# Kernel optimization log

Hardware: AMD Instinct MI355X
Metric: run time of the kernel (lower is better)

## Reference

```python
import jax, jax.numpy as jnp
import numpy as np

POINT_DIM, VOXEL_DIM, NUM_HEADS = 3, 256, 8
HEAD_DIM = VOXEL_DIM // NUM_HEADS


def _linear_params(key, fan_in, fan_out):
    kw, kb = jax.random.split(key)
    bound = 1.0 / np.sqrt(fan_in)
    W = jax.random.uniform(kw, (fan_out, fan_in), jnp.float32, -bound, bound)
    b = jax.random.uniform(kb, (fan_out,), jnp.float32, -bound, bound)
    return W, b


def setup_inputs() -> dict:
    key = jax.random.key(0)
    ks = jax.random.split(key, 7)
    points = jax.random.normal(ks[0], (2, 4096, POINT_DIM), jnp.float32)
    voxel_features = jax.random.normal(ks[1], (2, 2048, VOXEL_DIM), jnp.float32)
    Wp, bp = _linear_params(ks[2], POINT_DIM, VOXEL_DIM)
    Wq, bq = _linear_params(ks[3], VOXEL_DIM, VOXEL_DIM)
    Wk, bk = _linear_params(ks[4], VOXEL_DIM, VOXEL_DIM)
    Wv, bv = _linear_params(ks[5], VOXEL_DIM, VOXEL_DIM)
    Wf, bf = _linear_params(ks[6], VOXEL_DIM * 2, VOXEL_DIM)
    return {
        "points": points, "voxel_features": voxel_features,
        "Wp": Wp, "bp": bp, "Wq": Wq, "bq": bq,
        "Wk": Wk, "bk": bk, "Wv": Wv, "bv": bv,
        "Wf": Wf, "bf": bf,
    }


def reference(points, voxel_features, Wp, bp, Wq, bq, Wk, bk, Wv, bv, Wf, bf):
    B, N, _ = points.shape
    M = voxel_features.shape[1]
    # projections (torch Linear: x @ W.T + b)
    point_features = points @ Wp.T + bp                      # [B,N,D]
    q = (point_features @ Wq.T + bq).reshape(B, N, NUM_HEADS, HEAD_DIM)
    k = (voxel_features @ Wk.T + bk).reshape(B, M, NUM_HEADS, HEAD_DIM)
    v = (voxel_features @ Wv.T + bv).reshape(B, M, NUM_HEADS, HEAD_DIM)
    # attention scores [B,H,N,M]
    scale = 1.0 / np.sqrt(HEAD_DIM).astype(np.float32)
    attn = jnp.einsum('bnhd,bmhd->bhnm', q, k) * scale
    attn = jax.nn.softmax(attn, axis=-1)
    attended = jnp.einsum('bhnm,bmhd->bnhd', attn, v).reshape(B, N, VOXEL_DIM)
    fused = jnp.concatenate([point_features, attended], axis=-1) @ Wf.T + bf
    return fused
```

## Files before the change

### kernel.cpp

```cpp
#include <hip/hip_runtime.h>

#define B_ 2
#define N_ 4096
#define M_ 2048
#define D_ 256
#define H_ 8
#define DH_ 32
#define ROWS_ (B_*N_)
#define KVROWS_ (B_*M_)
#define PRE_ (0.17677669529663687f * 1.4426950408889634f)
#define CBASE_ 32.0f

typedef __attribute__((ext_vector_type(8))) short short8_t;
typedef __attribute__((ext_vector_type(4))) float float4_t;

#if defined(__has_builtin)
# if __has_builtin(__builtin_amdgcn_exp2f)
#  define EXP2F(x) __builtin_amdgcn_exp2f(x)
# else
#  define EXP2F(x) exp2f(x)
# endif
#else
# define EXP2F(x) exp2f(x)
#endif

__device__ __forceinline__ unsigned int rne_u(float f) {
    union { float f; unsigned int u; } c;
    c.f = f;
    return c.u + 0x7FFFu + ((c.u >> 16) & 1u);
}

__device__ __forceinline__ unsigned short f2us(float f) {
    return (unsigned short)(rne_u(f) >> 16);
}

__device__ __forceinline__ unsigned int pack2rn(float a, float b) {
    return __builtin_amdgcn_perm(rne_u(b), rne_u(a), 0x07060302u);
}

__device__ __forceinline__ unsigned int pack2tr(float a, float b) {
    union { float f; unsigned int u; } x, y;
    x.f = a; y.f = b;
    return __builtin_amdgcn_perm(y.u, x.u, 0x07060302u);
}

__device__ __forceinline__ short8_t cvt8(float4 a, float4 b) {
    union { unsigned int u[4]; short8_t s; } c;
    c.u[0] = pack2rn(a.x, a.y);
    c.u[1] = pack2rn(a.z, a.w);
    c.u[2] = pack2rn(b.x, b.y);
    c.u[3] = pack2rn(b.z, b.w);
    return c.s;
}

__device__ __forceinline__ int xcd_swz(int bid, int nwg) {
    const int cpx = nwg >> 3;
    return (bid & 7) * cpx + (bid >> 3);
}

template<int K, int NCOL>
__device__ __forceinline__ void stageB(const float* __restrict__ W, int col0,
                                       unsigned short* __restrict__ Bs, int tid)
{
    const int n = tid & (NCOL - 1), g = tid / NCOL;
    const int GROUPS = 256 / NCOL;
    const int CPT = (K / 8) / GROUPS;
    const float* src = W + (size_t)(col0 + n) * K + g * (K / GROUPS);
#pragma unroll
    for (int ci = 0; ci < CPT; ci++) {
        int logc = g * CPT + ci;
        int phys = logc ^ (n & 7);
        short8_t v = cvt8(*(const float4*)(src + ci * 8), *(const float4*)(src + ci * 8 + 4));
        *(short8_t*)(Bs + (size_t)n * K + phys * 8) = v;
    }
}

template<int K>
__device__ __forceinline__ short8_t readB(const unsigned short* __restrict__ Bs,
                                          int c, int l16, int quad, int k0)
{
    int phys = ((k0 >> 3) + quad) ^ (l16 & 7);
    return *(const short8_t*)(Bs + (size_t)(16 * c + l16) * K + phys * 8);
}

__global__ __launch_bounds__(256) void g_proj(
    const float* __restrict__ points, const float* __restrict__ voxel,
    const float* __restrict__ Wp, const float* __restrict__ bp,
    const float* __restrict__ Wq, const float* __restrict__ bq,
    const float* __restrict__ Wk, const float* __restrict__ bk,
    const float* __restrict__ Wv, const float* __restrict__ bv,
    unsigned short* __restrict__ pf_g, unsigned short* __restrict__ q_g,
    unsigned short* __restrict__ k_g, unsigned short* __restrict__ vt_g)
{
    const int tid = threadIdx.x;
    const int wave = tid >> 6, lane = tid & 63, quad = lane >> 4, l16 = lane & 15;

    __shared__ unsigned short Bs[64 * 256];
    __shared__ float Wp_lds[256 * 5];

    if (blockIdx.x < 512) {
        const int row0 = ((int)blockIdx.x >> 2) * 64;
        const int col0 = ((int)blockIdx.x & 3) * 64;
        stageB<256, 64>(Wq, col0, Bs, tid);
        Wp_lds[tid * 5 + 0] = Wp[tid * 3 + 0];
        Wp_lds[tid * 5 + 1] = Wp[tid * 3 + 1];
        Wp_lds[tid * 5 + 2] = Wp[tid * 3 + 2];
        Wp_lds[tid * 5 + 3] = bp[tid];
        __syncthreads();

        const int n = row0 + wave * 16 + l16;
        const float p0 = points[(size_t)n * 3 + 0];
        const float p1 = points[(size_t)n * 3 + 1];
        const float p2 = points[(size_t)n * 3 + 2];

        float4_t acc[4];
#pragma unroll
        for (int c = 0; c < 4; c++) acc[c] = (float4_t){0.f, 0.f, 0.f, 0.f};

#pragma unroll
        for (int k0 = 0; k0 < 256; k0 += 32) {
            float pf[8];
#pragma unroll
            for (int j = 0; j < 8; j++) {
                int c = k0 + quad * 8 + j;
                pf[j] = p0 * Wp_lds[c * 5 + 0] + p1 * Wp_lds[c * 5 + 1]
                      + p2 * Wp_lds[c * 5 + 2] + Wp_lds[c * 5 + 3];
            }
            short8_t af = cvt8(make_float4(pf[0], pf[1], pf[2], pf[3]),
                               make_float4(pf[4], pf[5], pf[6], pf[7]));
            if (col0 == 0)
                *(short8_t*)(pf_g + (size_t)n * D_ + k0 + quad * 8) = af;
#pragma unroll
            for (int c = 0; c < 4; c++)
                acc[c] = __builtin_amdgcn_mfma_f32_16x16x32_bf16(af, readB<256>(Bs, c, l16, quad, k0), acc[c], 0, 0, 0);
        }
#pragma unroll
        for (int c = 0; c < 4; c++) {
            int col = col0 + 16 * c + l16;
            float bb = bq[col];
#pragma unroll
            for (int r = 0; r < 4; r++) {
                int row = row0 + wave * 16 + quad * 4 + r;
                q_g[(size_t)row * D_ + col] = f2us((acc[c][r] + bb) * PRE_);
            }
        }
    } else {
        const int bid = (int)blockIdx.x - 512;
        const int row0 = (bid >> 2) * 64;
        const int col0 = (bid & 3) * 64;
        const float* arow = voxel + (size_t)(row0 + wave * 16 + l16) * D_;

        float4_t ak[4], av[4];
#pragma unroll
        for (int c = 0; c < 4; c++) {
            ak[c] = (float4_t){0.f, 0.f, 0.f, 0.f};
            av[c] = (float4_t){0.f, 0.f, 0.f, 0.f};
        }
        stageB<256, 64>(Wk, col0, Bs, tid);
        __syncthreads();
#pragma unroll
        for (int k0 = 0; k0 < 256; k0 += 32) {
            short8_t af = cvt8(*(const float4*)(arow + k0 + quad * 8),
                               *(const float4*)(arow + k0 + quad * 8 + 4));
#pragma unroll
            for (int c = 0; c < 4; c++)
                ak[c] = __builtin_amdgcn_mfma_f32_16x16x32_bf16(af, readB<256>(Bs, c, l16, quad, k0), ak[c], 0, 0, 0);
        }
        __syncthreads();
        stageB<256, 64>(Wv, col0, Bs, tid);
        __syncthreads();
#pragma unroll
        for (int k0 = 0; k0 < 256; k0 += 32) {
            short8_t af = cvt8(*(const float4*)(arow + k0 + quad * 8),
                               *(const float4*)(arow + k0 + quad * 8 + 4));
#pragma unroll
            for (int c = 0; c < 4; c++)
                av[c] = __builtin_amdgcn_mfma_f32_16x16x32_bf16(af, readB<256>(Bs, c, l16, quad, k0), av[c], 0, 0, 0);
        }
        const int b = row0 / M_;
        const int m0 = row0 - b * M_ + wave * 16 + quad * 4;
#pragma unroll
        for (int c = 0; c < 4; c++) {
            int col = col0 + 16 * c + l16;
            float bbk = bk[col], bbv = bv[col];
#pragma unroll
            for (int r = 0; r < 4; r++) {
                int row = row0 + wave * 16 + quad * 4 + r;
                k_g[(size_t)row * D_ + col] = f2us(ak[c][r] + bbk);
            }
            int h = col >> 5, dh = col & 31;
            unsigned int u0 = pack2rn(av[c][0] + bbv, av[c][1] + bbv);
            unsigned int u1 = pack2rn(av[c][2] + bbv, av[c][3] + bbv);
            *(uint2*)(vt_g + (size_t)((b * H_ + h) * DH_ + dh) * M_ + m0) = make_uint2(u0, u1);
        }
    }
}

__global__ __launch_bounds__(256) void k_attn6(
    const unsigned short* __restrict__ q_g,
    const unsigned short* __restrict__ k_g,
    const unsigned short* __restrict__ vt_g,
    unsigned short* __restrict__ att_g)
{
    const int tid = threadIdx.x;
    const int w = tid >> 6, lane = tid & 63, quad = lane >> 4, l16 = lane & 15;
    const int lbid = xcd_swz((int)blockIdx.x, B_ * H_ * (N_ / 64));
    const int nt = lbid & 63;
    const int bh = lbid >> 6;
    const int b = bh >> 3, h = bh & 7;
    const int n0 = nt * 64 + w * 16;

    __shared__ unsigned short Kt[2][64][40];
    __shared__ unsigned short Vt[2][32][72];
    __shared__ unsigned short Pb[4][16][64];

    short8_t qf = *(const short8_t*)(q_g + (size_t)(b * N_ + n0 + l16) * D_ + h * DH_ + quad * 8);

    float4_t od0 = {0.f, 0.f, 0.f, 0.f};
    float4_t od1 = {0.f, 0.f, 0.f, 0.f};
    float l_lane = 0.f;

    const unsigned short* kbase = k_g + (size_t)(b * M_) * D_ + h * DH_;
    const unsigned short* vbase = vt_g + (size_t)(bh * DH_) * M_;
    unsigned short* pb = &Pb[w][0][0];
    const int h7 = l16 & 7;
    const float4_t zc = {-CBASE_, -CBASE_, -CBASE_, -CBASE_};

    const int kr = tid >> 2, kc = tid & 3;
    const int vr = tid >> 3, vc = tid & 7;

    *(short8_t*)&Kt[0][kr][kc * 8] = *(const short8_t*)(kbase + (size_t)kr * D_ + kc * 8);
    *(short8_t*)&Vt[0][vr][vc * 8] = *(const short8_t*)(vbase + (size_t)vr * M_ + vc * 8);

    for (int s = 0; s < M_ / 64; s++) {
        __syncthreads();
        const int buf = s & 1;
        if (s + 1 < M_ / 64) {
            const int kv1 = (s + 1) * 64;
            *(short8_t*)&Kt[buf ^ 1][kr][kc * 8] =
                *(const short8_t*)(kbase + (size_t)(kv1 + kr) * D_ + kc * 8);
            *(short8_t*)&Vt[buf ^ 1][vr][vc * 8] =
                *(const short8_t*)(vbase + (size_t)vr * M_ + kv1 + vc * 8);
        }

        float4_t st[4];
#pragma unroll
        for (int t = 0; t < 4; t++) {
            short8_t kf = *(const short8_t*)&Kt[buf][16 * t + l16][quad * 8];
            st[t] = __builtin_amdgcn_mfma_f32_16x16x32_bf16(kf, qf, zc, 0, 0, 0);
        }

        float psum = 0.f;
#pragma unroll
        for (int t = 0; t < 4; t++) {
            float p0 = EXP2F(st[t][0]);
            float p1 = EXP2F(st[t][1]);
            float p2 = EXP2F(st[t][2]);
            float p3 = EXP2F(st[t][3]);
            psum += (p0 + p1) + (p2 + p3);
            unsigned int u0 = pack2tr(p0, p1);
            unsigned int u1 = pack2tr(p2, p3);
            int phys = (2 * t + (quad >> 1)) ^ h7;
            *(uint2*)(pb + l16 * 64 + phys * 8 + (quad & 1) * 4) = make_uint2(u0, u1);
        }
        l_lane += psum;

        short8_t pfa = *(const short8_t*)(pb + l16 * 64 + (quad ^ h7) * 8);
        short8_t pfb = *(const short8_t*)(pb + l16 * 64 + ((4 + quad) ^ h7) * 8);

        short8_t vf00 = *(const short8_t*)&Vt[buf][l16][quad * 8];
        short8_t vf01 = *(const short8_t*)&Vt[buf][l16][32 + quad * 8];
        short8_t vf10 = *(const short8_t*)&Vt[buf][16 + l16][quad * 8];
        short8_t vf11 = *(const short8_t*)&Vt[buf][16 + l16][32 + quad * 8];
        od0 = __builtin_amdgcn_mfma_f32_16x16x32_bf16(vf00, pfa, od0, 0, 0, 0);
        od0 = __builtin_amdgcn_mfma_f32_16x16x32_bf16(vf01, pfb, od0, 0, 0, 0);
        od1 = __builtin_amdgcn_mfma_f32_16x16x32_bf16(vf10, pfa, od1, 0, 0, 0);
        od1 = __builtin_amdgcn_mfma_f32_16x16x32_bf16(vf11, pfb, od1, 0, 0, 0);
    }

    l_lane += __shfl_xor(l_lane, 16);
    l_lane += __shfl_xor(l_lane, 32);
    const float inv = 1.0f / l_lane;

    unsigned short* ob = att_g + (size_t)(b * N_ + n0 + l16) * D_ + h * DH_;
    {
        unsigned int u0 = pack2rn(od0[0] * inv, od0[1] * inv);
        unsigned int u1 = pack2rn(od0[2] * inv, od0[3] * inv);
        *(uint2*)(ob + quad * 4) = make_uint2(u0, u1);
        unsigned int u2 = pack2rn(od1[0] * inv, od1[1] * inv);
        unsigned int u3 = pack2rn(od1[2] * inv, od1[3] * inv);
        *(uint2*)(ob + 16 + quad * 4) = make_uint2(u2, u3);
    }
}

__global__ __launch_bounds__(256) void g_fuse(
    const unsigned short* __restrict__ pf_g,
    const unsigned short* __restrict__ att_g,
    const float* __restrict__ Wf, const float* __restrict__ bfb,
    float* __restrict__ out)
{
    const int tid = threadIdx.x;
    const int wave = tid >> 6, lane = tid & 63, quad = lane >> 4, l16 = lane & 15;
    const int lbid = xcd_swz((int)blockIdx.x, (ROWS_ / 64) * 8);
    const int row0 = (lbid >> 3) * 64;
    const int col0 = (lbid & 7) * 32;

    __shared__ unsigned short Bs[32 * 512];

    stageB<512, 32>(Wf, col0, Bs, tid);
    __syncthreads();

    float4_t acc[2];
#pragma unroll
    for (int c = 0; c < 2; c++) acc[c] = (float4_t){0.f, 0.f, 0.f, 0.f};

    const size_t arow = (size_t)(row0 + wave * 16 + l16) * D_;
#pragma unroll
    for (int k0 = 0; k0 < 512; k0 += 32) {
        const unsigned short* xsrc = (k0 < 256) ? (pf_g + arow + k0) : (att_g + arow + (k0 - 256));
        short8_t af = *(const short8_t*)(xsrc + quad * 8);
#pragma unroll
        for (int c = 0; c < 2; c++)
            acc[c] = __builtin_amdgcn_mfma_f32_16x16x32_bf16(af, readB<512>(Bs, c, l16, quad, k0), acc[c], 0, 0, 0);
    }
#pragma unroll
    for (int c = 0; c < 2; c++) {
        int col = col0 + 16 * c + l16;
        float bb = bfb[col];
#pragma unroll
        for (int r = 0; r < 4; r++) {
            int row = row0 + wave * 16 + quad * 4 + r;
            out[(size_t)row * D_ + col] = acc[c][r] + bb;
        }
    }
}

extern "C" void kernel_launch(void* const* d_in, const int* in_sizes, int n_in,
                              void* d_out, int out_size, void* d_ws, size_t ws_size,
                              hipStream_t stream)
{
    const float* points = (const float*)d_in[0];
    const float* voxel  = (const float*)d_in[1];
    const float* Wp  = (const float*)d_in[2];
    const float* bp  = (const float*)d_in[3];
    const float* Wq  = (const float*)d_in[4];
    const float* bq  = (const float*)d_in[5];
    const float* Wk  = (const float*)d_in[6];
    const float* bk  = (const float*)d_in[7];
    const float* Wv  = (const float*)d_in[8];
    const float* bv  = (const float*)d_in[9];
    const float* Wf  = (const float*)d_in[10];
    const float* bfb = (const float*)d_in[11];
    float* out = (float*)d_out;

    unsigned short* ws = (unsigned short*)d_ws;
    unsigned short* pf_g  = ws;
    unsigned short* q_g   = pf_g  + (size_t)ROWS_ * D_;
    unsigned short* k_g   = q_g   + (size_t)ROWS_ * D_;
    unsigned short* vt_g  = k_g   + (size_t)KVROWS_ * D_;
    unsigned short* att_g = vt_g  + (size_t)KVROWS_ * D_;

    g_proj <<<dim3(768),  dim3(256), 0, stream>>>(points, voxel, Wp, bp, Wq, bq,
                                                  Wk, bk, Wv, bv, pf_g, q_g, k_g, vt_g);
    k_attn6<<<dim3(B_ * H_ * (N_ / 64)), dim3(256), 0, stream>>>(q_g, k_g, vt_g, att_g);
    g_fuse <<<dim3((ROWS_ / 64) * 8), dim3(256), 0, stream>>>(pf_g, att_g, Wf, bfb, out);
}
```

Measured before the change: 159.7 us.

## Fold point projection into Wq and Wf, compute q inside attention

```diff
diff --git a/kernel.cpp b/kernel.cpp
--- a/kernel.cpp
+++ b/kernel.cpp
@@ -58,14 +58,14 @@
     return (bid & 7) * cpx + (bid >> 3);
 }
 
-template<int K, int NCOL>
-__device__ __forceinline__ void stageB(const float* __restrict__ W, int col0,
-                                       unsigned short* __restrict__ Bs, int tid)
+template<int K, int NCOL, int LDSRC>
+__device__ __forceinline__ void stageB2(const float* __restrict__ W, int col0, int kof,
+                                        unsigned short* __restrict__ Bs, int tid)
 {
     const int n = tid & (NCOL - 1), g = tid / NCOL;
     const int GROUPS = 256 / NCOL;
     const int CPT = (K / 8) / GROUPS;
-    const float* src = W + (size_t)(col0 + n) * K + g * (K / GROUPS);
+    const float* src = W + (size_t)(col0 + n) * LDSRC + kof + g * (K / GROUPS);
 #pragma unroll
     for (int ci = 0; ci < CPT; ci++) {
         int logc = g * CPT + ci;
@@ -83,99 +83,47 @@
     return *(const short8_t*)(Bs + (size_t)(16 * c + l16) * K + phys * 8);
 }
 
-__global__ __launch_bounds__(256) void g_proj(
-    const float* __restrict__ points, const float* __restrict__ voxel,
+__global__ __launch_bounds__(256) void g_projkv(
+    const float* __restrict__ voxel,
     const float* __restrict__ Wp, const float* __restrict__ bp,
     const float* __restrict__ Wq, const float* __restrict__ bq,
     const float* __restrict__ Wk, const float* __restrict__ bk,
     const float* __restrict__ Wv, const float* __restrict__ bv,
-    unsigned short* __restrict__ pf_g, unsigned short* __restrict__ q_g,
-    unsigned short* __restrict__ k_g, unsigned short* __restrict__ vt_g)
+    const float* __restrict__ Wf, const float* __restrict__ bfb,
+    unsigned short* __restrict__ k_g, unsigned short* __restrict__ vt_g,
+    float* __restrict__ Wqc, float* __restrict__ Wfc)
 {
     const int tid = threadIdx.x;
     const int wave = tid >> 6, lane = tid & 63, quad = lane >> 4, l16 = lane & 15;
 
     __shared__ unsigned short Bs[64 * 256];
-    __shared__ float Wp_lds[256 * 5];
-
-    if (blockIdx.x < 512) {
-        const int row0 = ((int)blockIdx.x >> 2) * 64;
-        const int col0 = ((int)blockIdx.x & 3) * 64;
-        stageB<256, 64>(Wq, col0, Bs, tid);
-        Wp_lds[tid * 5 + 0] = Wp[tid * 3 + 0];
-        Wp_lds[tid * 5 + 1] = Wp[tid * 3 + 1];
-        Wp_lds[tid * 5 + 2] = Wp[tid * 3 + 2];
-        Wp_lds[tid * 5 + 3] = bp[tid];
-        __syncthreads();
-
-        const int n = row0 + wave * 16 + l16;
-        const float p0 = points[(size_t)n * 3 + 0];
-        const float p1 = points[(size_t)n * 3 + 1];
-        const float p2 = points[(size_t)n * 3 + 2];
-
-        float4_t acc[4];
-#pragma unroll
-        for (int c = 0; c < 4; c++) acc[c] = (float4_t){0.f, 0.f, 0.f, 0.f};
-
-#pragma unroll
-        for (int k0 = 0; k0 < 256; k0 += 32) {
-            float pf[8];
-#pragma unroll
-            for (int j = 0; j < 8; j++) {
-                int c = k0 + quad * 8 + j;
-                pf[j] = p0 * Wp_lds[c * 5 + 0] + p1 * Wp_lds[c * 5 + 1]
-                      + p2 * Wp_lds[c * 5 + 2] + Wp_lds[c * 5 + 3];
-            }
-            short8_t af = cvt8(make_float4(pf[0], pf[1], pf[2], pf[3]),
-                               make_float4(pf[4], pf[5], pf[6], pf[7]));
-            if (col0 == 0)
-                *(short8_t*)(pf_g + (size_t)n * D_ + k0 + quad * 8) = af;
-#pragma unroll
-            for (int c = 0; c < 4; c++)
-                acc[c] = __builtin_amdgcn_mfma_f32_16x16x32_bf16(af, readB<256>(Bs, c, l16, quad, k0), acc[c], 0, 0, 0);
-        }
-#pragma unroll
-        for (int c = 0; c < 4; c++) {
-            int col = col0 + 16 * c + l16;
-            float bb = bq[col];
-#pragma unroll
-            for (int r = 0; r < 4; r++) {
-                int row = row0 + wave * 16 + quad * 4 + r;
-                q_g[(size_t)row * D_ + col] = f2us((acc[c][r] + bb) * PRE_);
-            }
-        }
-    } else {
-        const int bid = (int)blockIdx.x - 512;
+    __shared__ unsigned short Bs2[64 * 256];
+
+    if (blockIdx.x < 256) {
+        const int bid = (int)blockIdx.x;
         const int row0 = (bid >> 2) * 64;
         const int col0 = (bid & 3) * 64;
         const float* arow = voxel + (size_t)(row0 + wave * 16 + l16) * D_;
 
+        stageB2<256, 64, 256>(Wk, col0, 0, Bs, tid);
+        stageB2<256, 64, 256>(Wv, col0, 0, Bs2, tid);
+
         float4_t ak[4], av[4];
 #pragma unroll
         for (int c = 0; c < 4; c++) {
             ak[c] = (float4_t){0.f, 0.f, 0.f, 0.f};
             av[c] = (float4_t){0.f, 0.f, 0.f, 0.f};
         }
-        stageB<256, 64>(Wk, col0, Bs, tid);
         __syncthreads();
 #pragma unroll
         for (int k0 = 0; k0 < 256; k0 += 32) {
             short8_t af = cvt8(*(const float4*)(arow + k0 + quad * 8),
                                *(const float4*)(arow + k0 + quad * 8 + 4));
 #pragma unroll
-            for (int c = 0; c < 4; c++)
-                ak[c] = __builtin_amdgcn_mfma_f32_16x16x32_bf16(af, readB<256>(Bs, c, l16, quad, k0), ak[c], 0, 0, 0);
-        }
-        __syncthreads();
-        stageB<256, 64>(Wv, col0, Bs, tid);
-        __syncthreads();
-#pragma unroll
-        for (int k0 = 0; k0 < 256; k0 += 32) {
-            short8_t af = cvt8(*(const float4*)(arow + k0 + quad * 8),
-                               *(const float4*)(arow + k0 + quad * 8 + 4));
-#pragma unroll
-            for (int c = 0; c < 4; c++)
-                av[c] = __builtin_amdgcn_mfma_f32_16x16x32_bf16(af, readB<256>(Bs, c, l16, quad, k0), av[c], 0, 0, 0);
+            for (int c = 0; c < 4; c++) {
+                ak[c] = __builtin_amdgcn_mfma_f32_16x16x32_bf16(af, readB<256>(Bs,  c, l16, quad, k0), ak[c], 0, 0, 0);
+                av[c] = __builtin_amdgcn_mfma_f32_16x16x32_bf16(af, readB<256>(Bs2, c, l16, quad, k0), av[c], 0, 0, 0);
+            }
         }
         const int b = row0 / M_;
         const int m0 = row0 - b * M_ + wave * 16 + quad * 4;
@@ -193,11 +141,39 @@
             unsigned int u1 = pack2rn(av[c][2] + bbv, av[c][3] + bbv);
             *(uint2*)(vt_g + (size_t)((b * H_ + h) * DH_ + dh) * M_ + m0) = make_uint2(u0, u1);
         }
-    }
-}
-
-__global__ __launch_bounds__(256) void k_attn6(
-    const unsigned short* __restrict__ q_g,
+    } else {
+        const int role = (int)blockIdx.x - 256;
+        float* wps = (float*)Bs;
+        *(float4*)(wps + tid * 4) = make_float4(Wp[tid * 3 + 0], Wp[tid * 3 + 1],
+                                                Wp[tid * 3 + 2], bp[tid]);
+        __syncthreads();
+        const int col = tid;
+        const float* wrow = role ? (Wf + (size_t)col * 512) : (Wq + (size_t)col * 256);
+        float a0 = 0.f, a1 = 0.f, a2 = 0.f, ab = 0.f;
+#pragma unroll 4
+        for (int d = 0; d < 256; d += 4) {
+            float4 wv = *(const float4*)(wrow + d);
+            float4 w0 = *(const float4*)(wps + (d + 0) * 4);
+            float4 w1 = *(const float4*)(wps + (d + 1) * 4);
+            float4 w2 = *(const float4*)(wps + (d + 2) * 4);
+            float4 w3 = *(const float4*)(wps + (d + 3) * 4);
+            a0 += wv.x * w0.x + wv.y * w1.x + wv.z * w2.x + wv.w * w3.x;
+            a1 += wv.x * w0.y + wv.y * w1.y + wv.z * w2.y + wv.w * w3.y;
+            a2 += wv.x * w0.z + wv.y * w1.z + wv.z * w2.z + wv.w * w3.z;
+            ab += wv.x * w0.w + wv.y * w1.w + wv.z * w2.w + wv.w * w3.w;
+        }
+        if (role == 0) {
+            *(float4*)(Wqc + (size_t)col * 4) =
+                make_float4(a0 * PRE_, a1 * PRE_, a2 * PRE_, (ab + bq[col]) * PRE_);
+        } else {
+            *(float4*)(Wfc + (size_t)col * 4) =
+                make_float4(a0, a1, a2, ab + bfb[col]);
+        }
+    }
+}
+
+__global__ __launch_bounds__(256) void k_attn7(
+    const float* __restrict__ points, const float* __restrict__ Wqc,
     const unsigned short* __restrict__ k_g,
     const unsigned short* __restrict__ vt_g,
     unsigned short* __restrict__ att_g)
@@ -214,52 +190,66 @@
     __shared__ unsigned short Vt[2][32][72];
     __shared__ unsigned short Pb[4][16][64];
 
-    short8_t qf = *(const short8_t*)(q_g + (size_t)(b * N_ + n0 + l16) * D_ + h * DH_ + quad * 8);
+    const unsigned short* kbase = k_g + (size_t)(b * M_) * D_ + h * DH_;
+    const unsigned short* vbase = vt_g + (size_t)(bh * DH_) * M_;
+
+    const int kr = tid >> 2, kc = tid & 3;
+    const int vr = tid >> 3, vc = tid & 7;
+
+    *(short8_t*)&Kt[0][kr][kc * 8] = *(const short8_t*)(kbase + (size_t)kr * D_ + kc * 8);
+    *(short8_t*)&Vt[0][vr][vc * 8] = *(const short8_t*)(vbase + (size_t)vr * M_ + vc * 8);
+
+    const size_t qrow = (size_t)(b * N_ + n0 + l16);
+    const float p0 = points[qrow * 3 + 0];
+    const float p1 = points[qrow * 3 + 1];
+    const float p2 = points[qrow * 3 + 2];
+    float q8[8];
+#pragma unroll
+    for (int j = 0; j < 8; j++) {
+        float4 wc = *(const float4*)(Wqc + (size_t)(h * DH_ + quad * 8 + j) * 4);
+        q8[j] = p0 * wc.x + p1 * wc.y + p2 * wc.z + wc.w;
+    }
+    short8_t qf = cvt8(make_float4(q8[0], q8[1], q8[2], q8[3]),
+                       make_float4(q8[4], q8[5], q8[6], q8[7]));
 
     float4_t od0 = {0.f, 0.f, 0.f, 0.f};
     float4_t od1 = {0.f, 0.f, 0.f, 0.f};
     float l_lane = 0.f;
 
-    const unsigned short* kbase = k_g + (size_t)(b * M_) * D_ + h * DH_;
-    const unsigned short* vbase = vt_g + (size_t)(bh * DH_) * M_;
     unsigned short* pb = &Pb[w][0][0];
     const int h7 = l16 & 7;
     const float4_t zc = {-CBASE_, -CBASE_, -CBASE_, -CBASE_};
 
-    const int kr = tid >> 2, kc = tid & 3;
-    const int vr = tid >> 3, vc = tid & 7;
-
-    *(short8_t*)&Kt[0][kr][kc * 8] = *(const short8_t*)(kbase + (size_t)kr * D_ + kc * 8);
-    *(short8_t*)&Vt[0][vr][vc * 8] = *(const short8_t*)(vbase + (size_t)vr * M_ + vc * 8);
-
     for (int s = 0; s < M_ / 64; s++) {
         __syncthreads();
         const int buf = s & 1;
-        if (s + 1 < M_ / 64) {
+        const bool more = (s + 1 < M_ / 64);
+        short8_t knext, vnext;
+        if (more) {
             const int kv1 = (s + 1) * 64;
-            *(short8_t*)&Kt[buf ^ 1][kr][kc * 8] =
-                *(const short8_t*)(kbase + (size_t)(kv1 + kr) * D_ + kc * 8);
-            *(short8_t*)&Vt[buf ^ 1][vr][vc * 8] =
-                *(const short8_t*)(vbase + (size_t)vr * M_ + kv1 + vc * 8);
+            knext = *(const short8_t*)(kbase + (size_t)(kv1 + kr) * D_ + kc * 8);
+            vnext = *(const short8_t*)(vbase + (size_t)vr * M_ + kv1 + vc * 8);
         }
 
         float4_t st[4];
+        __builtin_amdgcn_s_setprio(1);
 #pragma unroll
         for (int t = 0; t < 4; t++) {
             short8_t kf = *(const short8_t*)&Kt[buf][16 * t + l16][quad * 8];
             st[t] = __builtin_amdgcn_mfma_f32_16x16x32_bf16(kf, qf, zc, 0, 0, 0);
         }
+        __builtin_amdgcn_s_setprio(0);
 
         float psum = 0.f;
 #pragma unroll
         for (int t = 0; t < 4; t++) {
-            float p0 = EXP2F(st[t][0]);
-            float p1 = EXP2F(st[t][1]);
-            float p2 = EXP2F(st[t][2]);
-            float p3 = EXP2F(st[t][3]);
-            psum += (p0 + p1) + (p2 + p3);
-            unsigned int u0 = pack2tr(p0, p1);
-            unsigned int u1 = pack2tr(p2, p3);
+            float p0e = EXP2F(st[t][0]);
+            float p1e = EXP2F(st[t][1]);
+            float p2e = EXP2F(st[t][2]);
+            float p3e = EXP2F(st[t][3]);
+            psum += (p0e + p1e) + (p2e + p3e);
+            unsigned int u0 = pack2tr(p0e, p1e);
+            unsigned int u1 = pack2tr(p2e, p3e);
             int phys = (2 * t + (quad >> 1)) ^ h7;
             *(uint2*)(pb + l16 * 64 + phys * 8 + (quad & 1) * 4) = make_uint2(u0, u1);
         }
@@ -272,10 +262,17 @@
         short8_t vf01 = *(const short8_t*)&Vt[buf][l16][32 + quad * 8];
         short8_t vf10 = *(const short8_t*)&Vt[buf][16 + l16][quad * 8];
         short8_t vf11 = *(const short8_t*)&Vt[buf][16 + l16][32 + quad * 8];
+        __builtin_amdgcn_s_setprio(1);
         od0 = __builtin_amdgcn_mfma_f32_16x16x32_bf16(vf00, pfa, od0, 0, 0, 0);
         od0 = __builtin_amdgcn_mfma_f32_16x16x32_bf16(vf01, pfb, od0, 0, 0, 0);
         od1 = __builtin_amdgcn_mfma_f32_16x16x32_bf16(vf10, pfa, od1, 0, 0, 0);
         od1 = __builtin_amdgcn_mfma_f32_16x16x32_bf16(vf11, pfb, od1, 0, 0, 0);
+        __builtin_amdgcn_s_setprio(0);
+
+        if (more) {
+            *(short8_t*)&Kt[buf ^ 1][kr][kc * 8] = knext;
+            *(short8_t*)&Vt[buf ^ 1][vr][vc * 8] = vnext;
+        }
     }
 
     l_lane += __shfl_xor(l_lane, 16);
@@ -293,10 +290,10 @@
     }
 }
 
-__global__ __launch_bounds__(256) void g_fuse(
-    const unsigned short* __restrict__ pf_g,
+__global__ __launch_bounds__(256) void g_fuse2(
     const unsigned short* __restrict__ att_g,
-    const float* __restrict__ Wf, const float* __restrict__ bfb,
+    const float* __restrict__ points, const float* __restrict__ Wfc,
+    const float* __restrict__ Wf,
     float* __restrict__ out)
 {
     const int tid = threadIdx.x;
@@ -305,9 +302,9 @@
     const int row0 = (lbid >> 3) * 64;
     const int col0 = (lbid & 7) * 32;
 
-    __shared__ unsigned short Bs[32 * 512];
-
-    stageB<512, 32>(Wf, col0, Bs, tid);
+    __shared__ unsigned short Bs[32 * 256];
+
+    stageB2<256, 32, 512>(Wf, col0, 256, Bs, tid);
     __syncthreads();
 
     float4_t acc[2];
@@ -316,21 +313,29 @@
 
     const size_t arow = (size_t)(row0 + wave * 16 + l16) * D_;
 #pragma unroll
-    for (int k0 = 0; k0 < 512; k0 += 32) {
-        const unsigned short* xsrc = (k0 < 256) ? (pf_g + arow + k0) : (att_g + arow + (k0 - 256));
-        short8_t af = *(const short8_t*)(xsrc + quad * 8);
+    for (int k0 = 0; k0 < 256; k0 += 32) {
+        short8_t af = *(const short8_t*)(att_g + arow + k0 + quad * 8);
 #pragma unroll
         for (int c = 0; c < 2; c++)
-            acc[c] = __builtin_amdgcn_mfma_f32_16x16x32_bf16(af, readB<512>(Bs, c, l16, quad, k0), acc[c], 0, 0, 0);
+            acc[c] = __builtin_amdgcn_mfma_f32_16x16x32_bf16(af, readB<256>(Bs, c, l16, quad, k0), acc[c], 0, 0, 0);
+    }
+
+    const int rbase = row0 + wave * 16 + quad * 4;
+    float px[4], py[4], pz[4];
+#pragma unroll
+    for (int r = 0; r < 4; r++) {
+        px[r] = points[(size_t)(rbase + r) * 3 + 0];
+        py[r] = points[(size_t)(rbase + r) * 3 + 1];
+        pz[r] = points[(size_t)(rbase + r) * 3 + 2];
     }
 #pragma unroll
     for (int c = 0; c < 2; c++) {
         int col = col0 + 16 * c + l16;
-        float bb = bfb[col];
+        float4 wf = *(const float4*)(Wfc + (size_t)col * 4);
 #pragma unroll
         for (int r = 0; r < 4; r++) {
-            int row = row0 + wave * 16 + quad * 4 + r;
-            out[(size_t)row * D_ + col] = acc[c][r] + bb;
+            out[(size_t)(rbase + r) * D_ + col] =
+                acc[c][r] + px[r] * wf.x + py[r] * wf.y + pz[r] * wf.z + wf.w;
         }
     }
 }
@@ -353,15 +358,14 @@
     const float* bfb = (const float*)d_in[11];
     float* out = (float*)d_out;
 
-    unsigned short* ws = (unsigned short*)d_ws;
-    unsigned short* pf_g  = ws;
-    unsigned short* q_g   = pf_g  + (size_t)ROWS_ * D_;
-    unsigned short* k_g   = q_g   + (size_t)ROWS_ * D_;
-    unsigned short* vt_g  = k_g   + (size_t)KVROWS_ * D_;
-    unsigned short* att_g = vt_g  + (size_t)KVROWS_ * D_;
-
-    g_proj <<<dim3(768),  dim3(256), 0, stream>>>(points, voxel, Wp, bp, Wq, bq,
-                                                  Wk, bk, Wv, bv, pf_g, q_g, k_g, vt_g);
-    k_attn6<<<dim3(B_ * H_ * (N_ / 64)), dim3(256), 0, stream>>>(q_g, k_g, vt_g, att_g);
-    g_fuse <<<dim3((ROWS_ / 64) * 8), dim3(256), 0, stream>>>(pf_g, att_g, Wf, bfb, out);
-}
+    float* Wqc = (float*)d_ws;
+    float* Wfc = Wqc + 256 * 4;
+    unsigned short* k_g   = (unsigned short*)(Wfc + 256 * 4);
+    unsigned short* vt_g  = k_g  + (size_t)KVROWS_ * D_;
+    unsigned short* att_g = vt_g + (size_t)KVROWS_ * D_;
+
+    g_projkv<<<dim3(258),  dim3(256), 0, stream>>>(voxel, Wp, bp, Wq, bq, Wk, bk,
+                                                   Wv, bv, Wf, bfb, k_g, vt_g, Wqc, Wfc);
+    k_attn7 <<<dim3(B_ * H_ * (N_ / 64)), dim3(256), 0, stream>>>(points, Wqc, k_g, vt_g, att_g);
+    g_fuse2 <<<dim3((ROWS_ / 64) * 8), dim3(256), 0, stream>>>(att_g, points, Wfc, Wf, out);
+}
```

Result: faster. 143.4 us (-10.2%).
